# Kernel tuning notes

Measured on AMD Instinct MI355X. Metric: run time of the kernel, lower is better.

Reference implementation:

```python
import jax, jax.numpy as jnp
import numpy as np

N = 100000   # nodes
E = 3200000  # edges (before self-loops)
G = 256      # graphs in batch
IN_DIM, HID, OUT3 = 25, 64, 32


def setup_inputs() -> dict:
    key = jax.random.key(0)
    ks = jax.random.split(key, 13)
    def w(k, shape, fan_in):
        return jax.random.normal(k, shape, jnp.float32) * (1.0 / np.sqrt(fan_in))
    return {
        "x": jax.random.normal(ks[0], (N, IN_DIM), jnp.float32),
        "edge_index": jax.random.randint(ks[1], (2, E), 0, N, dtype=jnp.int32),
        "batch": jnp.sort(jax.random.randint(ks[2], (N,), 0, G, dtype=jnp.int32)),
        "W1": w(ks[3], (IN_DIM, HID), IN_DIM), "b1": jnp.zeros((HID,), jnp.float32),
        "W2": w(ks[4], (HID, HID), HID),       "b2": jnp.zeros((HID,), jnp.float32),
        "W3": w(ks[5], (HID, OUT3), HID),      "b3": jnp.zeros((OUT3,), jnp.float32),
        "Wh1": w(ks[6], (OUT3, 32), OUT3),     "bh1": jnp.zeros((32,), jnp.float32),
        "Wh2": w(ks[7], (32, 1), 32),          "bh2": jnp.zeros((1,), jnp.float32),
    }


def _gcn_layer(x, W, b, src, dst, num_nodes):
    # GCNConv: h = W^T x; out_i = sum_j norm_ij * h_j (+ self-loop), norm = d_i^-1/2 d_j^-1/2
    h = x @ W  # [N, F_out]
    ones = jnp.ones(src.shape[0], h.dtype)
    deg = jax.ops.segment_sum(ones, dst, num_segments=num_nodes)  # includes self-loops -> >= 1
    dinv = jax.lax.rsqrt(jnp.maximum(deg, 1.0))
    norm = dinv[src] * dinv[dst]                       # [E+N]
    msgs = h[src] * norm[:, None]                       # gather + scale
    out = jax.ops.segment_sum(msgs, dst, num_segments=num_nodes)  # scatter-add
    return out + b


def reference(x, edge_index, batch, W1, b1, W2, b2, W3, b3, Wh1, bh1, Wh2, bh2):
    n = x.shape[0]
    loops = jnp.arange(n, dtype=edge_index.dtype)
    src = jnp.concatenate([edge_index[0], loops])  # add self-loops
    dst = jnp.concatenate([edge_index[1], loops])

    h = jax.nn.relu(_gcn_layer(x, W1, b1, src, dst, n))
    h = jax.nn.relu(_gcn_layer(h, W2, b2, src, dst, n))
    h = jax.nn.relu(_gcn_layer(h, W3, b3, src, dst, n))

    # global mean pool over graphs
    counts = jax.ops.segment_sum(jnp.ones(n, h.dtype), batch, num_segments=G)
    g = jax.ops.segment_sum(h, batch, num_segments=G) / jnp.maximum(counts, 1.0)[:, None]

    y = jax.nn.relu(g @ Wh1 + bh1) @ Wh2 + bh2  # [G, 1]
    return y.squeeze(-1)
```

## Files before the change

### kernel.cpp

```cpp
#include <hip/hip_runtime.h>
#include <hip/hip_fp16.h>


#define IN_DIM 25
#define HID 64
#define OUT3 32
#define BK_LOG 6
#define BK_NODES 64
#define CB_LOG 8
#define NCB 512
#define EPB1 8192
#define BCAP2 10240
#define RNG_LOG 14
#define NR 8
#define NKEY2 2048

__global__ __launch_bounds__(256) void bucket_hist(const int* __restrict__ dst,
                                                   int* __restrict__ bhist, int nE) {
    __shared__ int h[NCB];
    for (int i = threadIdx.x; i < NCB; i += 256) h[i] = 0;
    __syncthreads();
    int e0 = blockIdx.x * 8192;
    int cnt = min(8192, nE - e0);
    for (int i = threadIdx.x; i < cnt; i += 256)
        atomicAdd(&h[(unsigned)dst[e0 + i] >> CB_LOG], 1);
    __syncthreads();
    for (int i = threadIdx.x; i < NCB; i += 256)
        if (h[i]) atomicAdd(&bhist[i], h[i]);
}

__global__ __launch_bounds__(256) void bucket_scan(const int* __restrict__ bhist,
                                                   int* __restrict__ bbase,
                                                   int* __restrict__ cursor,
                                                   int nb, int nE) {
    __shared__ int s4[256];
    int t = threadIdx.x;
    int v[2]; int sum = 0;
#pragma unroll
    for (int j = 0; j < 2; ++j) {
        int b = 2 * t + j;
        v[j] = (b < nb) ? bhist[b] : 0;
        sum += v[j];
    }
    s4[t] = sum;
    __syncthreads();
    for (int off = 1; off < 256; off <<= 1) {
        int mine = s4[t];
        int add = (t >= off) ? s4[t - off] : 0;
        __syncthreads();
        s4[t] = mine + add;
        __syncthreads();
    }
    int run = s4[t] - sum;
#pragma unroll
    for (int j = 0; j < 2; ++j) {
        int b = 2 * t + j;
        if (b < nb) { bbase[b] = run; cursor[b] = run; }
        run += v[j];
    }
    if (t == 0) bbase[nb] = nE;
}

__global__ __launch_bounds__(256) void partition_kernel(
        const int* __restrict__ src, const int* __restrict__ dst,
        int* __restrict__ cursor, unsigned int* __restrict__ ebuf, int nE) {
    __shared__ int lh[NCB];
    __shared__ int lrun[NCB];
    int t = threadIdx.x;
    int e0 = blockIdx.x * EPB1;
    int cnt = min(EPB1, nE - e0);
    for (int i = t; i < NCB; i += 256) lh[i] = 0;
    __syncthreads();
    for (int i = t; i < cnt; i += 256)
        atomicAdd(&lh[(unsigned)dst[e0 + i] >> CB_LOG], 1);
    __syncthreads();
    for (int b = t; b < NCB; b += 256) {
        int v = lh[b];
        lh[b] = 0;
        if (v > 0) lrun[b] = atomicAdd(&cursor[b], v);
    }
    __syncthreads();
    for (int i = t; i < cnt; i += 256) {
        int d = dst[e0 + i];
        int s = src[e0 + i];
        int cb = (unsigned)d >> CB_LOG;
        int lp = atomicAdd(&lh[cb], 1);
        unsigned int w = ((unsigned)(d & 255) << 17) | (unsigned)s;
        ebuf[lrun[cb] + lp] = w;
    }
}

__global__ __launch_bounds__(256) void coarse_sort_kernel(
        unsigned int* __restrict__ ebuf, const int* __restrict__ bbase,
        float* __restrict__ dinv, int* __restrict__ gp64, int* __restrict__ gp32,
        int nN) {
    int cb = blockIdx.x;
    int node_lo = cb << CB_LOG;
    int base = bbase[cb];
    int cnt = bbase[cb + 1] - base;
    if (cnt > BCAP2) cnt = BCAP2;
    __shared__ unsigned int in[BCAP2];
    __shared__ int h[NKEY2];
    __shared__ int sc[NKEY2 + 1];
    __shared__ int swp[256];
    int t = threadIdx.x;
    for (int i = t; i < cnt; i += 256) in[i] = ebuf[base + i];
    for (int i = t; i < NKEY2; i += 256) h[i] = 0;
    __syncthreads();
    for (int i = t; i < cnt; i += 256) {
        unsigned int w = in[i];
        int kk = (int)(((w >> 23) & 3u) << 9) | (int)(((w >> RNG_LOG) & 7u) << 6)
               | (int)((w >> 17) & 63u);
        atomicAdd(&h[kk], 1);
    }
    __syncthreads();
    int v[8]; int sum = 0;
#pragma unroll
    for (int j = 0; j < 8; ++j) { v[j] = h[8 * t + j]; sum += v[j]; }
    swp[t] = sum;
    __syncthreads();
    for (int off = 1; off < 256; off <<= 1) {
        int mine = swp[t];
        int add = (t >= off) ? swp[t - off] : 0;
        __syncthreads();
        swp[t] = mine + add;
        __syncthreads();
    }
    int run = swp[t] - sum;
#pragma unroll
    for (int j = 0; j < 8; ++j) { sc[8 * t + j] = run; run += v[j]; }
    if (t == 255) sc[NKEY2] = run;
    __syncthreads();
    {
        int fb = t >> 6, idx = t & 63;
        gp64[(cb * 4 + fb) * 65 + idx] = base + sc[(fb << 9) | (idx << 3)];
    }
    if (t < 4) gp64[(cb * 4 + t) * 65 + 64] = base + sc[(t + 1) << 9];
    for (int i = t; i < 512; i += 256) {
        int fb = i >> 7, idx = i & 127;
        gp32[(cb * 4 + fb) * 129 + idx] = base + sc[(fb << 9) | (idx << 2)];
    }
    if (t < 4) gp32[(cb * 4 + t) * 129 + 128] = base + sc[(t + 1) << 9];
    {
        int node = node_lo + t;
        if (node < nN) {
            int fb = t >> 6, dl = t & 63;
            int deg = 0;
#pragma unroll
            for (int r = 0; r < NR; ++r) {
                int k = (fb << 9) | (r << 6) | dl;
                deg += sc[k + 1] - sc[k];
            }
            dinv[node] = rsqrtf((float)deg + 1.0f);
        }
    }
    for (int i = t; i < NKEY2; i += 256) h[i] = 0;
    __syncthreads();
    for (int i = t; i < cnt; i += 256) {
        unsigned int w = in[i];
        int kk = (int)(((w >> 23) & 3u) << 9) | (int)(((w >> RNG_LOG) & 7u) << 6)
               | (int)((w >> 17) & 63u);
        int lp = atomicAdd(&h[kk], 1);
        ebuf[base + sc[kk] + lp] = w & 0x7FFFFFu;
    }
}

__global__ void padx_kernel(const float* __restrict__ x, const float* __restrict__ dinv,
                            __half* __restrict__ xp, int n) {
    int i = blockIdx.x * 256 + threadIdx.x;
    if (i < n * 16) {
        int node = i >> 4, c2 = (i & 15) * 2;
        float s = dinv[node];
        float v0 = (c2     < IN_DIM) ? x[(size_t)node * IN_DIM + c2    ] * s : 0.f;
        float v1 = (c2 + 1 < IN_DIM) ? x[(size_t)node * IN_DIM + c2 + 1] * s : 0.f;
        *(__half2*)&xp[(size_t)node * 32 + c2] = __floats2half2_rn(v0, v1);
    }
}

__global__ void padw_kernel(const float* __restrict__ W1, float* __restrict__ W1p) {
    int i = blockIdx.x * 256 + threadIdx.x;
    if (i < 32 * HID) {
        int r = i >> 6, c = i & 63;
        W1p[i] = (r < IN_DIM) ? W1[r * HID + c] : 0.f;
    }
}

template<int INF, int OUTF, bool ACT, bool SCALE, bool INH, bool OUTH>
__global__ __launch_bounds__(256) void gemm_kernel(
        const void* __restrict__ in, const float* __restrict__ W,
        const float* __restrict__ bias, const float* __restrict__ dinv,
        void* __restrict__ out, int n) {
    constexpr int TPN = OUTF / 4;
    constexpr int NPB = 256 / TPN;
    constexpr int LDK = INF + 4;
    __shared__ float sW[INF * OUTF];
    __shared__ float sIn[NPB][LDK];
    for (int i = threadIdx.x; i < INF * OUTF; i += 256) sW[i] = W[i];
    int node0 = blockIdx.x * NPB;
    for (int i = threadIdx.x; i < NPB * INF; i += 256) {
        int ln = i / INF, k = i % INF;
        int node = node0 + ln;
        float vv = 0.f;
        if (node < n) {
            if (INH) vv = __half2float(((const __half*)in)[(size_t)node * INF + k]);
            else     vv = ((const float*)in)[(size_t)node * INF + k];
        }
        sIn[ln][k] = vv;
    }
    __syncthreads();
    int g   = threadIdx.x / TPN;
    int of0 = (threadIdx.x % TPN) * 4;
    int node = node0 + g;
    float4 acc = make_float4(0.f, 0.f, 0.f, 0.f);
#pragma unroll
    for (int k = 0; k < INF; ++k) {
        float aj = sIn[g][k];
        const float4 wv = *(const float4*)&sW[k * OUTF + of0];
        acc.x += aj * wv.x; acc.y += aj * wv.y;
        acc.z += aj * wv.z; acc.w += aj * wv.w;
    }
    if (ACT) {
        const float4 bv = *(const float4*)&bias[of0];
        acc.x = fmaxf(acc.x + bv.x, 0.f);
        acc.y = fmaxf(acc.y + bv.y, 0.f);
        acc.z = fmaxf(acc.z + bv.z, 0.f);
        acc.w = fmaxf(acc.w + bv.w, 0.f);
    }
    if (node < n) {
        if (SCALE || OUTH) {
            float s = SCALE ? dinv[node] : 1.f;
            union { __half2 h[2]; uint2 u; } pk;
            pk.h[0] = __floats2half2_rn(acc.x * s, acc.y * s);
            pk.h[1] = __floats2half2_rn(acc.z * s, acc.w * s);
            *(uint2*)((__half*)out + (size_t)node * OUTF + of0) = pk.u;
        } else {
            *(float4*)((float*)out + (size_t)node * OUTF + of0) = acc;
        }
    }
}

template<int F, bool ACT, bool OUTH>
__global__ __launch_bounds__(256, 6) void gatherp_kernel(
        const __half* __restrict__ hp, const float* __restrict__ dinv,
        const int* __restrict__ gp, const unsigned int* __restrict__ eb,
        const float* __restrict__ bias, void* __restrict__ aggv, int n) {
    constexpr int LPN = F / 2;
    constexpr int G   = 256 / LPN;
    constexpr int GPB = NR * G + 1;
    __shared__ float acc[(BK_NODES + 1) * F];
    int b = blockIdx.x, t = threadIdx.x;
    int node_lo = b << BK_LOG;
    for (int i = t; i < BK_NODES * LPN; i += 256) {
        int ln = i / LPN, c2 = (i % LPN) * 2;
        int node = node_lo + ln;
        float2 v = make_float2(0.f, 0.f);
        if (node < n)
            v = __half22float2(*(const __half2*)&hp[(size_t)node * F + c2]);
        acc[ln * F + c2] = v.x;
        acc[ln * F + c2 + 1] = v.y;
    }
    __syncthreads();
    int g  = t / LPN;
    int c2 = (t % LPN) * 2;
    float ax = 0.f, ay = 0.f;
    int cur = BK_NODES;
    for (int r = 0; r < NR; ++r) {
        int e  = gp[b * GPB + r * G + g];
        int e1 = gp[b * GPB + r * G + g + 1];
        for (; e + 8 <= e1; e += 8) {
            unsigned int w[8];
#pragma unroll
            for (int u = 0; u < 8; ++u) w[u] = eb[e + u];
            float2 v[8];
#pragma unroll
            for (int u = 0; u < 8; ++u)
                v[u] = __half22float2(
                    *(const __half2*)&hp[(size_t)(w[u] & 0x1FFFFu) * F + c2]);
#pragma unroll
            for (int u = 0; u < 8; ++u) {
                int dl = (int)(w[u] >> 17);
                if (dl != cur) {
                    acc[cur * F + c2]     += ax;
                    acc[cur * F + c2 + 1] += ay;
                    ax = 0.f; ay = 0.f; cur = dl;
                }
                ax += v[u].x; ay += v[u].y;
            }
        }
        for (; e < e1; ++e) {
            unsigned int w = eb[e];
            float2 v = __half22float2(
                *(const __half2*)&hp[(size_t)(w & 0x1FFFFu) * F + c2]);
            int dl = (int)(w >> 17);
            if (dl != cur) {
                acc[cur * F + c2]     += ax;
                acc[cur * F + c2 + 1] += ay;
                ax = 0.f; ay = 0.f; cur = dl;
            }
            ax += v.x; ay += v.y;
        }
        acc[cur * F + c2]     += ax;
        acc[cur * F + c2 + 1] += ay;
        ax = 0.f; ay = 0.f; cur = BK_NODES;
        __syncthreads();
    }
    for (int i = t; i < BK_NODES * LPN; i += 256) {
        int ln = i / LPN, cc = (i % LPN) * 2;
        int node = node_lo + ln;
        if (node < n) {
            float s = dinv[node];
            float rx = acc[ln * F + cc] * s;
            float ry = acc[ln * F + cc + 1] * s;
            if (ACT) {
                rx = fmaxf(rx + bias[cc], 0.f);
                ry = fmaxf(ry + bias[cc + 1], 0.f);
            }
            if (OUTH) {
                union { __half2 h; unsigned int u; } o;
                o.h = __floats2half2_rn(rx, ry);
                __builtin_nontemporal_store(o.u,
                    (unsigned int*)((__half*)aggv + (size_t)node * F + cc));
            } else {
                union { float2 f; unsigned long long u; } o;
                o.f = make_float2(rx, ry);
                __builtin_nontemporal_store(o.u,
                    (unsigned long long*)((float*)aggv + (size_t)node * F + cc));
            }
        }
    }
}

__global__ __launch_bounds__(256) void pool_kernel(
        const float* __restrict__ h3, const int* __restrict__ batch,
        int n, float* __restrict__ pool) {
    int g = blockIdx.x;
    int lo = 0, hi = n;
    while (lo < hi) { int m = (lo + hi) >> 1; if (batch[m] < g) lo = m + 1; else hi = m; }
    int s = lo;
    hi = n;
    while (lo < hi) { int m = (lo + hi) >> 1; if (batch[m] < g + 1) lo = m + 1; else hi = m; }
    int e = lo;
    constexpr int F = OUT3;
    int ln = threadIdx.x / F;
    int f  = threadIdx.x % F;
    float acc = 0.f;
    for (int i = s + ln; i < e; i += 8)
        acc += h3[(size_t)i * F + f];
    __shared__ float red[8][F];
    red[ln][f] = acc;
    __syncthreads();
    if (ln == 0) {
        float t = 0.f;
#pragma unroll
        for (int j = 0; j < 8; ++j) t += red[j][f];
        float cnt = (float)((e - s) > 0 ? (e - s) : 1);
        pool[g * F + f] = t / cnt;
    }
}

__global__ __launch_bounds__(256) void head_kernel(
        const float* __restrict__ pool, const float* __restrict__ Wh1,
        const float* __restrict__ bh1, const float* __restrict__ Wh2,
        const float* __restrict__ bh2, float* __restrict__ out) {
    __shared__ float sW1[32 * 32];
    __shared__ float sb1[32];
    __shared__ float sW2[32];
    int t = threadIdx.x;
    for (int i = t; i < 1024; i += 256) sW1[i] = Wh1[i];
    if (t < 32) { sb1[t] = bh1[t]; sW2[t] = Wh2[t]; }
    __syncthreads();
    int g = t;
    float y = bh2[0];
    const float* p = &pool[g * 32];
#pragma unroll 4
    for (int j = 0; j < 32; ++j) {
        float a = sb1[j];
#pragma unroll
        for (int k = 0; k < 32; ++k) a += p[k] * sW1[k * 32 + j];
        y += fmaxf(a, 0.f) * sW2[j];
    }
    out[g] = y;
}

extern "C" void kernel_launch(void* const* d_in, const int* in_sizes, int n_in,
                              void* d_out, int out_size, void* d_ws, size_t ws_size,
                              hipStream_t stream) {
    const float* x    = (const float*)d_in[0];
    const int*   ei   = (const int*)  d_in[1];
    const int*   batch= (const int*)  d_in[2];
    const float* W1   = (const float*)d_in[3];
    const float* b1   = (const float*)d_in[4];
    const float* W2   = (const float*)d_in[5];
    const float* b2   = (const float*)d_in[6];
    const float* W3   = (const float*)d_in[7];
    const float* b3   = (const float*)d_in[8];
    const float* Wh1  = (const float*)d_in[9];
    const float* bh1  = (const float*)d_in[10];
    const float* Wh2  = (const float*)d_in[11];
    const float* bh2  = (const float*)d_in[12];
    float* out = (float*)d_out;

    const int N = in_sizes[0] / IN_DIM;
    const int E = in_sizes[1] / 2;
    const int* src = ei;
    const int* dst = ei + E;
    const int NB = (N + BK_NODES - 1) >> BK_LOG;

    char* base = (char*)d_ws;
    unsigned int* ebuf = (unsigned int*)base;       base += (size_t)E * 4;
    int*   bhist   = (int*)base;                    base += (size_t)NCB * 4;
    int*   bbase   = (int*)base;                    base += (size_t)(NCB + 1) * 4;
    int*   cursor  = (int*)base;                    base += (size_t)NCB * 4;
    int*   gp64    = (int*)base;                    base += (size_t)(NCB * 4) * 65 * 4;
    int*   gp32    = (int*)base;                    base += (size_t)(NCB * 4) * 129 * 4;
    float* dinv    = (float*)base;                  base += (size_t)N * 4;
    float* W1p     = (float*)base;                  base += (size_t)32 * HID * 4;
    float* bufA    = (float*)base;                  base += (size_t)N * HID * 4;
    float* bufB    = (float*)base;                  base += (size_t)N * HID * 4;
    float* pool    = (float*)base;

    hipMemsetAsync(bhist, 0, (size_t)NCB * sizeof(int), stream);
    bucket_hist<<<(E + 8191) / 8192, 256, 0, stream>>>(dst, bhist, E);
    bucket_scan<<<1, 256, 0, stream>>>(bhist, bbase, cursor, NCB, E);
    partition_kernel<<<(E + EPB1 - 1) / EPB1, 256, 0, stream>>>(src, dst, cursor, ebuf, E);
    coarse_sort_kernel<<<NCB, 256, 0, stream>>>(ebuf, bbase, dinv, gp64, gp32, N);

    padx_kernel<<<((size_t)N * 16 + 255) / 256, 256, 0, stream>>>(x, dinv, (__half*)bufB, N);
    padw_kernel<<<(32 * HID + 255) / 256, 256, 0, stream>>>(W1, W1p);
    gatherp_kernel<32, false, true><<<NB, 256, 0, stream>>>((const __half*)bufB, dinv, gp32, ebuf, nullptr, bufA, N);
    gemm_kernel<32, HID, true, false, true, true><<<(N + 15) / 16, 256, 0, stream>>>(bufA, W1p, b1, nullptr, bufB, N);

    gemm_kernel<HID, HID, false, true, true, false><<<(N + 15) / 16, 256, 0, stream>>>(bufB, W2, nullptr, dinv, bufA, N);
    gatherp_kernel<64, true, true><<<NB, 256, 0, stream>>>((const __half*)bufA, dinv, gp64, ebuf, b2, bufB, N);

    gemm_kernel<HID, OUT3, false, true, true, false><<<(N + 31) / 32, 256, 0, stream>>>(bufB, W3, nullptr, dinv, bufA, N);
    gatherp_kernel<32, true, false><<<NB, 256, 0, stream>>>((const __half*)bufA, dinv, gp32, ebuf, b3, bufB, N);

    pool_kernel<<<256, 256, 0, stream>>>(bufB, batch, N, pool);
    head_kernel<<<1, 256, 0, stream>>>(pool, Wh1, bh1, Wh2, bh2, out);
}
```

Measured before the change: 461.9 us.

## Fuse neighbor aggregation with following dense GEMM per node bucket

Adds a fused kernel that performs the sparse gather-aggregate for a 64-node bucket into shared memory, applies normalization/bias/ReLU, and then multiplies by the next layer's weight matrix held in shared memory. It replaces gather+gemm pairs for layer 1 and for layer2-aggregation+layer3-transform. This removes intermediate round trips of N x F activations through global memory and two kernel launches. In exchange, shared memory per block grows (weights plus padded accumulator), which may reduce occupancy, and the GEMM runs on scalar FMAs inside the gather kernel.

```diff
diff --git a/kernel.cpp b/kernel.cpp
--- a/kernel.cpp
+++ b/kernel.cpp
@@ -239,6 +239,118 @@
     }
 }
 
+template<int F, int OUTF, bool GB, bool GEMM_ACT, bool GEMM_SCALE>
+__global__ __launch_bounds__(256, 6) void fused_kernel(
+        const __half* __restrict__ hp, const float* __restrict__ dinv,
+        const int* __restrict__ gp, const unsigned int* __restrict__ eb,
+        const float* __restrict__ gbias, const float* __restrict__ W,
+        const float* __restrict__ gemm_bias, __half* __restrict__ out, int n) {
+    constexpr int LPN = F / 2;
+    constexpr int G   = 256 / LPN;
+    constexpr int GPB = NR * G + 1;
+    constexpr int LDA = F + 1;
+    __shared__ float acc[(BK_NODES + 1) * LDA];
+    __shared__ float sW[F * OUTF];
+    int b = blockIdx.x, t = threadIdx.x;
+    int node_lo = b << BK_LOG;
+    for (int i = t; i < F * OUTF; i += 256) sW[i] = W[i];
+    for (int i = t; i < BK_NODES * LPN; i += 256) {
+        int ln = i / LPN, c2 = (i % LPN) * 2;
+        int node = node_lo + ln;
+        float2 v = make_float2(0.f, 0.f);
+        if (node < n)
+            v = __half22float2(*(const __half2*)&hp[(size_t)node * F + c2]);
+        acc[ln * LDA + c2] = v.x;
+        acc[ln * LDA + c2 + 1] = v.y;
+    }
+    __syncthreads();
+    int g  = t / LPN;
+    int c2 = (t % LPN) * 2;
+    float ax = 0.f, ay = 0.f;
+    int cur = BK_NODES;
+    for (int r = 0; r < NR; ++r) {
+        int e  = gp[b * GPB + r * G + g];
+        int e1 = gp[b * GPB + r * G + g + 1];
+        for (; e + 8 <= e1; e += 8) {
+            unsigned int w[8];
+#pragma unroll
+            for (int u = 0; u < 8; ++u) w[u] = eb[e + u];
+            float2 v[8];
+#pragma unroll
+            for (int u = 0; u < 8; ++u)
+                v[u] = __half22float2(
+                    *(const __half2*)&hp[(size_t)(w[u] & 0x1FFFFu) * F + c2]);
+#pragma unroll
+            for (int u = 0; u < 8; ++u) {
+                int dl = (int)(w[u] >> 17);
+                if (dl != cur) {
+                    acc[cur * LDA + c2]     += ax;
+                    acc[cur * LDA + c2 + 1] += ay;
+                    ax = 0.f; ay = 0.f; cur = dl;
+                }
+                ax += v[u].x; ay += v[u].y;
+            }
+        }
+        for (; e < e1; ++e) {
+            unsigned int w = eb[e];
+            float2 v = __half22float2(
+                *(const __half2*)&hp[(size_t)(w & 0x1FFFFu) * F + c2]);
+            int dl = (int)(w >> 17);
+            if (dl != cur) {
+                acc[cur * LDA + c2]     += ax;
+                acc[cur * LDA + c2 + 1] += ay;
+                ax = 0.f; ay = 0.f; cur = dl;
+            }
+            ax += v.x; ay += v.y;
+        }
+        acc[cur * LDA + c2]     += ax;
+        acc[cur * LDA + c2 + 1] += ay;
+        ax = 0.f; ay = 0.f; cur = BK_NODES;
+        __syncthreads();
+    }
+    for (int i = t; i < BK_NODES * F; i += 256) {
+        int ln = i / F, c = i & (F - 1);
+        int node = node_lo + ln;
+        if (node < n) {
+            float a = acc[ln * LDA + c] * dinv[node];
+            if (GB) a = fmaxf(a + gbias[c], 0.f);
+            acc[ln * LDA + c] = a;
+        }
+    }
+    __syncthreads();
+    constexpr int TPN = OUTF / 4;
+    constexpr int NPB = 256 / TPN;
+    int gg  = t / TPN;
+    int of0 = (t % TPN) * 4;
+#pragma unroll
+    for (int p = 0; p < BK_NODES; p += NPB) {
+        int ln = p + gg;
+        int node = node_lo + ln;
+        float4 o = make_float4(0.f, 0.f, 0.f, 0.f);
+#pragma unroll 8
+        for (int k = 0; k < F; ++k) {
+            float a = acc[ln * LDA + k];
+            const float4 w4 = *(const float4*)&sW[k * OUTF + of0];
+            o.x += a * w4.x; o.y += a * w4.y;
+            o.z += a * w4.z; o.w += a * w4.w;
+        }
+        if (GEMM_ACT) {
+            const float4 bv = *(const float4*)&gemm_bias[of0];
+            o.x = fmaxf(o.x + bv.x, 0.f);
+            o.y = fmaxf(o.y + bv.y, 0.f);
+            o.z = fmaxf(o.z + bv.z, 0.f);
+            o.w = fmaxf(o.w + bv.w, 0.f);
+        }
+        if (node < n) {
+            float s = GEMM_SCALE ? dinv[node] : 1.f;
+            union { __half2 h[2]; uint2 u; } pk;
+            pk.h[0] = __floats2half2_rn(o.x * s, o.y * s);
+            pk.h[1] = __floats2half2_rn(o.z * s, o.w * s);
+            *(uint2*)&out[(size_t)node * OUTF + of0] = pk.u;
+        }
+    }
+}
+
 template<int F, bool ACT, bool OUTH>
 __global__ __launch_bounds__(256, 6) void gatherp_kernel(
         const __half* __restrict__ hp, const float* __restrict__ dinv,
@@ -427,14 +539,17 @@
 
     padx_kernel<<<((size_t)N * 16 + 255) / 256, 256, 0, stream>>>(x, dinv, (__half*)bufB, N);
     padw_kernel<<<(32 * HID + 255) / 256, 256, 0, stream>>>(W1, W1p);
-    gatherp_kernel<32, false, true><<<NB, 256, 0, stream>>>((const __half*)bufB, dinv, gp32, ebuf, nullptr, bufA, N);
-    gemm_kernel<32, HID, true, false, true, true><<<(N + 15) / 16, 256, 0, stream>>>(bufA, W1p, b1, nullptr, bufB, N);
-
-    gemm_kernel<HID, HID, false, true, true, false><<<(N + 15) / 16, 256, 0, stream>>>(bufB, W2, nullptr, dinv, bufA, N);
-    gatherp_kernel<64, true, true><<<NB, 256, 0, stream>>>((const __half*)bufA, dinv, gp64, ebuf, b2, bufB, N);
-
-    gemm_kernel<HID, OUT3, false, true, true, false><<<(N + 31) / 32, 256, 0, stream>>>(bufB, W3, nullptr, dinv, bufA, N);
-    gatherp_kernel<32, true, false><<<NB, 256, 0, stream>>>((const __half*)bufA, dinv, gp32, ebuf, b3, bufB, N);
+    fused_kernel<32, HID, false, true, false><<<NB, 256, 0, stream>>>(
+        (const __half*)bufB, dinv, gp32, ebuf, nullptr, W1p, b1, (__half*)bufA, N);
+
+    gemm_kernel<HID, HID, false, true, true, false><<<(N + 15) / 16, 256, 0, stream>>>(
+        bufA, W2, nullptr, dinv, bufB, N);
+
+    fused_kernel<HID, OUT3, true, false, true><<<NB, 256, 0, stream>>>(
+        (const __half*)bufB, dinv, gp64, ebuf, b2, W3, nullptr, (__half*)bufA, N);
+
+    gatherp_kernel<32, true, false><<<NB, 256, 0, stream>>>(
+        (const __half*)bufA, dinv, gp32, ebuf, b3, bufB, N);
 
     pool_kernel<<<256, 256, 0, stream>>>(bufB, batch, N, pool);
     head_kernel<<<1, 256, 0, stream>>>(pool, Wh1, bh1, Wh2, bh2, out);
```

New measurement: 472.1 us. 2.2% more time.
